# Optimization experiments

Hardware: AMD Instinct MI355X
Metric: run time of the kernel (lower is better)

## Reference

```python
import jax, jax.numpy as jnp
import numpy as np

B = 8192          # batch
D = 256           # feature_dim
H = 64            # num attention heads
HD = D // H       # head_dim = 4
NC, NB, NF, NT = 2048, 2048, 512, 768
NCLS = 26
EPS = 1e-5


def _linear_params(k, out_d, in_d):
    s = 1.0 / np.sqrt(in_d)
    kw, kb = jax.random.split(k)
    W = jax.random.uniform(kw, (out_d, in_d), minval=-s, maxval=s, dtype=jnp.float32)
    b = jax.random.uniform(kb, (out_d,), minval=-s, maxval=s, dtype=jnp.float32)
    return W, b


def setup_inputs() -> dict:
    key = jax.random.key(0)
    ks = jax.random.split(key, 16)
    inp = {
        'x_context': jax.random.normal(ks[0], (B, NC), dtype=jnp.float32),
        'x_body':    jax.random.normal(ks[1], (B, NB), dtype=jnp.float32),
        'x_face':    jax.random.normal(ks[2], (B, NF), dtype=jnp.float32),
        'x_text':    jax.random.normal(ks[3], (B, NT), dtype=jnp.float32),
    }
    inp['Wc'], inp['bc'] = _linear_params(ks[4], D, NC)
    inp['Wb'], inp['bb'] = _linear_params(ks[5], D, NB)
    inp['Wf'], inp['bf'] = _linear_params(ks[6], D, NF)
    inp['Wt'], inp['bt'] = _linear_params(ks[7], D, NT)
    # MultiheadAttention packed in-proj (3D x D) and out-proj
    inp['in_w'], inp['in_b'] = _linear_params(ks[8], 3 * D, D)
    inp['out_w'], inp['out_b'] = _linear_params(ks[9], D, D)
    # gate MLP
    inp['Wg1'], inp['bg1'] = _linear_params(ks[10], D, D)
    inp['Wg2'], inp['bg2'] = _linear_params(ks[11], 1, D)
    # fusion head
    inp['W1'], inp['b1'] = _linear_params(ks[12], D, 4 * D)
    inp['gamma'] = jnp.ones((D,), dtype=jnp.float32)
    inp['beta'] = jnp.zeros((D,), dtype=jnp.float32)
    inp['W2'], inp['b2'] = _linear_params(ks[13], NCLS, D)
    return inp


def reference(x_context, x_body, x_face, x_text,
              Wc, bc, Wb, bb, Wf, bf, Wt, bt,
              in_w, in_b, out_w, out_b,
              Wg1, bg1, Wg2, bg2,
              W1, b1, gamma, beta, W2, b2):
    # per-modality projections -> [B, 4, D]
    f = jnp.stack([
        x_context @ Wc.T + bc,
        x_body    @ Wb.T + bb,
        x_face    @ Wf.T + bf,
        x_text    @ Wt.T + bt,
    ], axis=1)
    bsz = f.shape[0]

    # MultiheadAttention with seq_len=1 per token: softmax over a single key
    Wq, Wk, Wv = jnp.split(in_w, 3, axis=0)
    bq, bk, bv = jnp.split(in_b, 3)
    q = (f @ Wq.T + bq).reshape(bsz, 4, H, HD)
    k = (f @ Wk.T + bk).reshape(bsz, 4, H, HD)
    v = (f @ Wv.T + bv).reshape(bsz, 4, H, HD)
    scores = jnp.sum(q * k, axis=-1, keepdims=True) / np.sqrt(HD)  # [B,4,H,1]
    w = jax.nn.softmax(scores, axis=-1)                            # == 1 (single key)
    attn = (w * v).reshape(bsz, 4, D)
    self_out = attn @ out_w.T + out_b                              # [B,4,D]

    # cross attention: with seq_len=1 the output depends only on key/value,
    # so each (query i, key 3-j) call equals the self-style output of modality 3-j;
    # combining over the 4 key variants reduces to the mean over modalities.
    cross = jnp.mean(self_out, axis=1, keepdims=True)              # [B,1,D]

    gate = jax.nn.sigmoid(jax.nn.relu(self_out @ Wg1.T + bg1) @ Wg2.T + bg2)  # [B,4,1]
    combined = gate * self_out + (1.0 - gate) * cross              # [B,4,D]

    h = combined.reshape(bsz, 4 * D) @ W1.T + b1                   # [B,D]
    # BatchNorm1d (training-mode batch statistics, biased variance)
    mu = jnp.mean(h, axis=0)
    var = jnp.var(h, axis=0)
    h = (h - mu) / jnp.sqrt(var + EPS) * gamma + beta
    h = jax.nn.relu(h)                                             # dropout = identity (eval)
    return h @ W2.T + b2                                           # [B,26]
```

## Files before the change

### kernel.cpp

```cpp
#include <hip/hip_runtime.h>
#include <math.h>

typedef __attribute__((ext_vector_type(8))) short bf16x8;
typedef __attribute__((ext_vector_type(4))) float f32x4;
typedef unsigned short u16;
typedef unsigned int u32;

#define BSZ   8192
#define BN_EPS 1e-5f

__device__ inline u16 f2bf(float x) {
    u32 u = __float_as_uint(x);
    u32 r = (u + 0x7FFFu + ((u >> 16) & 1u)) >> 16;
    return (u16)r;
}
__device__ inline float bf2f_lo(u32 p) { return __uint_as_float(p << 16); }
__device__ inline float bf2f_hi(u32 p) { return __uint_as_float(p & 0xFFFF0000u); }

__device__ inline void async_g2l(const void* g, void* l) {
    __builtin_amdgcn_global_load_lds(
        (const __attribute__((address_space(1))) void*)g,
        (__attribute__((address_space(3))) void*)l, 16, 0, 0);
}

__global__ __launch_bounds__(256)
void wvo_kernel(const float* __restrict__ in_w, const float* __restrict__ in_b,
                const float* __restrict__ out_w, const float* __restrict__ out_b,
                float* __restrict__ wvo, float* __restrict__ bvo)
{
    const int i = blockIdx.x;
    const int j = threadIdx.x;
    const float* Wv = in_w + 512 * 256;
    float s = 0.f;
#pragma unroll 8
    for (int k = 0; k < 256; ++k)
        s = fmaf(out_w[i * 256 + k], Wv[k * 256 + j], s);
    wvo[i * 256 + j] = s;
    if (i == 0) {
        const float* bv = in_b + 512;
        float t = 0.f;
        for (int k = 0; k < 256; ++k)
            t = fmaf(out_w[j * 256 + k], bv[k], t);
        bvo[j] = t + out_b[j];
    }
}

__global__ __launch_bounds__(256)
void cvt_weights(const float* __restrict__ wvo, const float* __restrict__ Wc,
                 const float* __restrict__ Wb,  const float* __restrict__ Wf,
                 const float* __restrict__ Wt,  const float* __restrict__ Wg1,
                 const float* __restrict__ W1f, u16* __restrict__ dst)
{
    int gid = blockIdx.x * 256 + threadIdx.x;
    const float* src; u16* d; int loc;
    if      (gid <   8192) { src = wvo; d = dst + 0;       loc = gid; }
    else if (gid <  73728) { src = Wc;  d = dst + 65536;   loc = gid - 8192; }
    else if (gid < 139264) { src = Wb;  d = dst + 589824;  loc = gid - 73728; }
    else if (gid < 155648) { src = Wf;  d = dst + 1114112; loc = gid - 139264; }
    else if (gid < 180224) { src = Wt;  d = dst + 1245184; loc = gid - 155648; }
    else if (gid < 188416) { src = Wg1; d = dst + 1441792; loc = gid - 180224; }
    else                   { src = W1f; d = dst + 1507328; loc = gid - 188416; }
    const float4 v0 = *(const float4*)(src + (size_t)loc * 8);
    const float4 v1 = *(const float4*)(src + (size_t)loc * 8 + 4);
    uint4 o;
    o.x = (u32)f2bf(v0.x) | ((u32)f2bf(v0.y) << 16);
    o.y = (u32)f2bf(v0.z) | ((u32)f2bf(v0.w) << 16);
    o.z = (u32)f2bf(v1.x) | ((u32)f2bf(v1.y) << 16);
    o.w = (u32)f2bf(v1.z) | ((u32)f2bf(v1.w) << 16);
    *(uint4*)(d + (size_t)loc * 8) = o;
}

__global__ __launch_bounds__(256)
void gemm_proj(const float* __restrict__ A0, const float* __restrict__ A1,
               const float* __restrict__ A2, const float* __restrict__ A3,
               const u16* __restrict__ Wp0, const u16* __restrict__ Wp1,
               const u16* __restrict__ Wp2, const u16* __restrict__ Wp3,
               const float* __restrict__ b0, const float* __restrict__ b1,
               const float* __restrict__ b2, const float* __restrict__ b3,
               u16* __restrict__ fb)
{
    __shared__ u16 As[2][4096];
    __shared__ u16 Bs[2][16384];
    const int m = blockIdx.y;
    const float* A  = (m == 0) ? A0 : (m == 1) ? A1 : (m == 2) ? A2 : A3;
    const u16* Wp   = (m == 0) ? Wp0 : (m == 1) ? Wp1 : (m == 2) ? Wp2 : Wp3;
    const float* bi = (m == 0) ? b0 : (m == 1) ? b1 : (m == 2) ? b2 : b3;
    const int K     = (m == 0) ? 2048 : (m == 1) ? 2048 : (m == 2) ? 512 : 768;
    const int nt = K >> 6;

    const int t = threadIdx.x;
    const int w = t >> 6, l = t & 63;
    const int bm = blockIdx.x * 64;
    const int arow = t >> 2, akq = t & 3;

    float4 rA[4], rB[4];
    auto loadA = [&](int k0, float4* r) {
        const float* g = A + (size_t)(bm + arow) * K + k0 + akq * 16;
#pragma unroll
        for (int q = 0; q < 4; ++q) r[q] = *(const float4*)(g + q * 4);
    };
    auto writeA = [&](int buf, const float4* r) {
        bf16x8 p0, p1;
        p0[0] = (short)f2bf(r[0].x); p0[1] = (short)f2bf(r[0].y);
        p0[2] = (short)f2bf(r[0].z); p0[3] = (short)f2bf(r[0].w);
        p0[4] = (short)f2bf(r[1].x); p0[5] = (short)f2bf(r[1].y);
        p0[6] = (short)f2bf(r[1].z); p0[7] = (short)f2bf(r[1].w);
        p1[0] = (short)f2bf(r[2].x); p1[1] = (short)f2bf(r[2].y);
        p1[2] = (short)f2bf(r[2].z); p1[3] = (short)f2bf(r[2].w);
        p1[4] = (short)f2bf(r[3].x); p1[5] = (short)f2bf(r[3].y);
        p1[6] = (short)f2bf(r[3].z); p1[7] = (short)f2bf(r[3].w);
        char* abw = (char*)As[buf];
        *(bf16x8*)(abw + arow * 128 + (((akq * 2 + 0) ^ (arow & 7)) << 4)) = p0;
        *(bf16x8*)(abw + arow * 128 + (((akq * 2 + 1) ^ (arow & 7)) << 4)) = p1;
    };
    auto issueB = [&](int k0, int buf) {
#pragma unroll
        for (int it = 0; it < 8; ++it) {
            const int n  = it * 32 + w * 8 + (l >> 3);
            const int ch = (l & 7) ^ (n & 7);
            async_g2l(Wp + (size_t)n * K + k0 + ch * 8, Bs[buf] + it * 2048 + w * 512);
        }
    };

    f32x4 acc[4][4];
    const f32x4 z = {0.f, 0.f, 0.f, 0.f};
#pragma unroll
    for (int i = 0; i < 4; ++i)
#pragma unroll
        for (int j = 0; j < 4; ++j) acc[i][j] = z;

    auto compute = [&](const char* abr, const char* bbr) {
#pragma unroll
        for (int kk = 0; kk < 2; ++kk) {
            bf16x8 af[4], bq[4];
            const int ch = kk * 4 + (l >> 4);
#pragma unroll
            for (int i = 0; i < 4; ++i) {
                const int fr = i * 16 + (l & 15);
                af[i] = *(const bf16x8*)(abr + fr * 128 + ((ch ^ (fr & 7)) << 4));
            }
#pragma unroll
            for (int j = 0; j < 4; ++j) {
                const int n = w * 64 + j * 16 + (l & 15);
                bq[j] = *(const bf16x8*)(bbr + n * 128 + ((ch ^ (n & 7)) << 4));
            }
#pragma unroll
            for (int i = 0; i < 4; ++i)
#pragma unroll
                for (int j = 0; j < 4; ++j)
                    acc[i][j] = __builtin_amdgcn_mfma_f32_16x16x32_bf16(
                        af[i], bq[j], acc[i][j], 0, 0, 0);
        }
    };

    loadA(0, rA);
    writeA(0, rA);
    issueB(0, 0);
    loadA(64, rB);
    issueB(64, 1);
    loadA(128, rA);
    asm volatile("s_waitcnt vmcnt(16) lgkmcnt(0)" ::: "memory");
    __builtin_amdgcn_sched_barrier(0);
    __builtin_amdgcn_s_barrier();

    for (int t0 = 0; t0 < nt; t0 += 2) {
        compute((const char*)As[0], (const char*)Bs[0]);
        writeA(1, rB);
        __builtin_amdgcn_s_barrier();
        if (t0 + 3 < nt) {
            loadA((t0 + 3) * 64, rB);
            issueB((t0 + 2) * 64, 0);
            asm volatile("s_waitcnt vmcnt(12) lgkmcnt(0)" ::: "memory");
        } else if (t0 + 2 < nt) {
            issueB((t0 + 2) * 64, 0);
            asm volatile("s_waitcnt vmcnt(8) lgkmcnt(0)" ::: "memory");
        } else {
            asm volatile("s_waitcnt vmcnt(0) lgkmcnt(0)" ::: "memory");
        }
        __builtin_amdgcn_sched_barrier(0);
        __builtin_amdgcn_s_barrier();

        compute((const char*)As[1], (const char*)Bs[1]);
        if (t0 + 2 < nt) writeA(0, rA);
        __builtin_amdgcn_s_barrier();
        if (t0 + 4 < nt) {
            loadA((t0 + 4) * 64, rA);
            issueB((t0 + 3) * 64, 1);
            asm volatile("s_waitcnt vmcnt(12) lgkmcnt(0)" ::: "memory");
        } else if (t0 + 3 < nt) {
            issueB((t0 + 3) * 64, 1);
            asm volatile("s_waitcnt vmcnt(8) lgkmcnt(0)" ::: "memory");
        } else {
            asm volatile("s_waitcnt vmcnt(0) lgkmcnt(0)" ::: "memory");
        }
        __builtin_amdgcn_sched_barrier(0);
        __builtin_amdgcn_s_barrier();
    }

#pragma unroll
    for (int j = 0; j < 4; ++j) {
        const int col = w * 64 + j * 16 + (l & 15);
        const float bv = bi[col];
#pragma unroll
        for (int i = 0; i < 4; ++i)
#pragma unroll
            for (int r = 0; r < 4; ++r) {
                const int rt = i * 16 + ((l >> 4) << 2) + r;
                fb[((size_t)(bm + rt) * 4 + m) * 256 + col] = f2bf(acc[i][j][r] + bv);
            }
    }
}

__global__ __launch_bounds__(256)
void fused_sgc(const u16* __restrict__ fb, const u16* __restrict__ wvo_bf,
               const float* __restrict__ bvo,
               const u16* __restrict__ wg1_bf, const float* __restrict__ bg1,
               const float* __restrict__ wg2, const float* __restrict__ bg2,
               u16* __restrict__ comb)
{
    __shared__ u16 FS[8192];
    __shared__ u16 Bs[2][8192];
    __shared__ float gp[4][32];
    __shared__ float gate_s[32];
    const int t = threadIdx.x, w = t >> 6, l = t & 63;
    const int bm = blockIdx.x * 32;
    char* const fs = (char*)FS;

#pragma unroll
    for (int it = 0; it < 4; ++it) {
        const int r0 = (w * 4 + it) * 2;
        const int row = r0 + (l >> 5);
        const int ch = (l & 31) ^ (row & 7);
        async_g2l(fb + (size_t)(bm + row) * 256 + ch * 8, FS + r0 * 256);
    }
    auto issueB = [&](const u16* Wp, int k0, int buf) {
#pragma unroll
        for (int it = 0; it < 4; ++it) {
            const int n0 = (w * 4 + it) * 16;
            async_g2l(Wp + (size_t)(n0 + (l >> 2)) * 256 + k0 + (l & 3) * 8,
                      Bs[buf] + n0 * 32);
        }
    };
    issueB(wvo_bf, 0, 0);
    __syncthreads();

    const f32x4 z = {0.f, 0.f, 0.f, 0.f};

    f32x4 acc[2][4];
#pragma unroll
    for (int i = 0; i < 2; ++i)
#pragma unroll
        for (int j = 0; j < 4; ++j) acc[i][j] = z;

    for (int ks = 0; ks < 8; ++ks) {
        const int cur = ks & 1;
        if (ks < 7) issueB(wvo_bf, (ks + 1) * 32, cur ^ 1);
        else        issueB(wg1_bf, 0, 0);
        bf16x8 af[2], bq[4];
#pragma unroll
        for (int i = 0; i < 2; ++i) {
            const int row = i * 16 + (l & 15);
            af[i] = *(const bf16x8*)(fs + row * 512 +
                      (((ks * 4 + (l >> 4)) ^ (row & 7)) << 4));
        }
#pragma unroll
        for (int j = 0; j < 4; ++j)
            bq[j] = *(const bf16x8*)((char*)Bs[cur] +
                      (w * 64 + j * 16 + (l & 15)) * 64 + (l >> 4) * 16);
#pragma unroll
        for (int i = 0; i < 2; ++i)
#pragma unroll
            for (int j = 0; j < 4; ++j)
                acc[i][j] = __builtin_amdgcn_mfma_f32_16x16x32_bf16(
                    af[i], bq[j], acc[i][j], 0, 0, 0);
        __syncthreads();
    }

#pragma unroll
    for (int j = 0; j < 4; ++j) {
        const int col = w * 64 + j * 16 + (l & 15);
        const float bv = bvo[col];
#pragma unroll
        for (int i = 0; i < 2; ++i)
#pragma unroll
            for (int r = 0; r < 4; ++r) {
                const int rt = i * 16 + ((l >> 4) << 2) + r;
                *(u16*)(fs + rt * 512 + (((col >> 3) ^ (rt & 7)) << 4) + (col & 7) * 2)
                    = f2bf(acc[i][j][r] + bv);
            }
    }
    __syncthreads();

    f32x4 g2[2][4];
#pragma unroll
    for (int i = 0; i < 2; ++i)
#pragma unroll
        for (int j = 0; j < 4; ++j) g2[i][j] = z;

    for (int ks = 0; ks < 8; ++ks) {
        const int cur = ks & 1;
        if (ks < 7) issueB(wg1_bf, (ks + 1) * 32, cur ^ 1);
        bf16x8 af[2], bq[4];
#pragma unroll
        for (int i = 0; i < 2; ++i) {
            const int row = i * 16 + (l & 15);
            af[i] = *(const bf16x8*)(fs + row * 512 +
                      (((ks * 4 + (l >> 4)) ^ (row & 7)) << 4));
        }
#pragma unroll
        for (int j = 0; j < 4; ++j)
            bq[j] = *(const bf16x8*)((char*)Bs[cur] +
                      (w * 64 + j * 16 + (l & 15)) * 64 + (l >> 4) * 16);
#pragma unroll
        for (int i = 0; i < 2; ++i)
#pragma unroll
            for (int j = 0; j < 4; ++j)
                g2[i][j] = __builtin_amdgcn_mfma_f32_16x16x32_bf16(
                    af[i], bq[j], g2[i][j], 0, 0, 0);
        __syncthreads();
    }

    {
        float s[2][4];
#pragma unroll
        for (int i = 0; i < 2; ++i)
#pragma unroll
            for (int r = 0; r < 4; ++r) s[i][r] = 0.f;
#pragma unroll
        for (int j = 0; j < 4; ++j) {
            const int col = w * 64 + j * 16 + (l & 15);
            const float bv = bg1[col], wv = wg2[col];
#pragma unroll
            for (int i = 0; i < 2; ++i)
#pragma unroll
                for (int r = 0; r < 4; ++r)
                    s[i][r] += fmaxf(g2[i][j][r] + bv, 0.f) * wv;
        }
#pragma unroll
        for (int off = 1; off < 16; off <<= 1)
#pragma unroll
            for (int i = 0; i < 2; ++i)
#pragma unroll
                for (int r = 0; r < 4; ++r)
                    s[i][r] += __shfl_xor(s[i][r], off);
        if ((l & 15) == 0) {
#pragma unroll
            for (int i = 0; i < 2; ++i)
#pragma unroll
                for (int r = 0; r < 4; ++r)
                    gp[w][i * 16 + ((l >> 4) << 2) + r] = s[i][r];
        }
    }
    __syncthreads();
    if (t < 32) {
        const float g = gp[0][t] + gp[1][t] + gp[2][t] + gp[3][t] + bg2[0];
        gate_s[t] = 1.f / (1.f + expf(-g));
    }
    __syncthreads();

    u32* const comb32 = (u32*)comb;
    const int p2 = t & 127;
    const int gh = t >> 7;
#pragma unroll
    for (int gg = 0; gg < 4; ++gg) {
        const int g = gh * 4 + gg;
        const int d0 = p2 * 2;
        float lo4[4], hi4[4], gv[4];
#pragma unroll
        for (int mm = 0; mm < 4; ++mm) {
            const int row = g * 4 + mm;
            const u32 v = *(const u32*)(fs + row * 512 +
                            (((d0 >> 3) ^ (row & 7)) << 4) + (d0 & 7) * 2);
            lo4[mm] = bf2f_lo(v); hi4[mm] = bf2f_hi(v);
            gv[mm] = gate_s[g * 4 + mm];
        }
        const float cl = 0.25f * (lo4[0] + lo4[1] + lo4[2] + lo4[3]);
        const float ch = 0.25f * (hi4[0] + hi4[1] + hi4[2] + hi4[3]);
#pragma unroll
        for (int mm = 0; mm < 4; ++mm) {
            const float ol = gv[mm] * lo4[mm] + (1.f - gv[mm]) * cl;
            const float oh = gv[mm] * hi4[mm] + (1.f - gv[mm]) * ch;
            comb32[(size_t)(bm + g * 4 + mm) * 128 + p2] =
                (u32)f2bf(ol) | ((u32)f2bf(oh) << 16);
        }
    }
}

__global__ __launch_bounds__(256)
void gemm_w1ps(const u16* __restrict__ combp, const u16* __restrict__ w1p,
               const float* __restrict__ b1p, float* __restrict__ h,
               float* __restrict__ psum, float* __restrict__ psq)
{
    __shared__ u16 As[2][1024];
    __shared__ u16 Bs[2][8192];
    const int t = threadIdx.x, w = t >> 6, l = t & 63;
    const int bm = blockIdx.x * 32;
    const int nt = 32;

    auto issueA = [&](int k0, int buf) {
        if (w < 2) {
            const int r0 = w * 16;
            async_g2l(combp + (size_t)(bm + r0 + (l >> 2)) * 1024 + k0 + (l & 3) * 8,
                      As[buf] + r0 * 32);
        }
    };
    auto issueB = [&](int k0, int buf) {
#pragma unroll
        for (int it = 0; it < 4; ++it) {
            const int n0 = (w * 4 + it) * 16;
            async_g2l(w1p + (size_t)(n0 + (l >> 2)) * 1024 + k0 + (l & 3) * 8,
                      Bs[buf] + n0 * 32);
        }
    };

    f32x4 acc[2][4];
    const f32x4 z = {0.f, 0.f, 0.f, 0.f};
#pragma unroll
    for (int i = 0; i < 2; ++i)
#pragma unroll
        for (int j = 0; j < 4; ++j) acc[i][j] = z;

    issueA(0, 0);
    issueB(0, 0);
    __syncthreads();

    for (int t0 = 0; t0 < nt; ++t0) {
        const int cur = t0 & 1;
        if (t0 + 1 < nt) { issueA((t0 + 1) * 32, cur ^ 1); issueB((t0 + 1) * 32, cur ^ 1); }
        const char* ab = (const char*)As[cur];
        const char* bb = (const char*)Bs[cur];
        bf16x8 af[2], bq[4];
#pragma unroll
        for (int i = 0; i < 2; ++i)
            af[i] = *(const bf16x8*)(ab + (i * 16 + (l & 15)) * 64 + (l >> 4) * 16);
#pragma unroll
        for (int j = 0; j < 4; ++j)
            bq[j] = *(const bf16x8*)(bb + (w * 64 + j * 16 + (l & 15)) * 64 + (l >> 4) * 16);
#pragma unroll
        for (int i = 0; i < 2; ++i)
#pragma unroll
            for (int j = 0; j < 4; ++j)
                acc[i][j] = __builtin_amdgcn_mfma_f32_16x16x32_bf16(
                    af[i], bq[j], acc[i][j], 0, 0, 0);
        __syncthreads();
    }

#pragma unroll
    for (int j = 0; j < 4; ++j) {
        const int col = w * 64 + j * 16 + (l & 15);
        const float bv = b1p[col];
        float cs = 0.f, cq = 0.f;
#pragma unroll
        for (int i = 0; i < 2; ++i)
#pragma unroll
            for (int r = 0; r < 4; ++r) {
                const int rt = i * 16 + ((l >> 4) << 2) + r;
                const float v = acc[i][j][r] + bv;
                h[(size_t)(bm + rt) * 256 + col] = v;
                cs += v;
                cq = fmaf(v, v, cq);
            }
        cs += __shfl_xor(cs, 16); cq += __shfl_xor(cq, 16);
        cs += __shfl_xor(cs, 32); cq += __shfl_xor(cq, 32);
        if ((l >> 4) == 0) {
            psum[blockIdx.x * 256 + col] = cs;
            psq[blockIdx.x * 256 + col]  = cq;
        }
    }
}

__global__ __launch_bounds__(256)
void bn_fin(const float* __restrict__ psum, const float* __restrict__ psq,
            const float* __restrict__ gamma, const float* __restrict__ beta,
            float* __restrict__ scale, float* __restrict__ shift)
{
    const int d = threadIdx.x;
    float s = 0.f, q = 0.f;
#pragma unroll 8
    for (int p = 0; p < 256; ++p) { s += psum[p * 256 + d]; q += psq[p * 256 + d]; }
    const float mu  = s * (1.f / BSZ);
    const float var = q * (1.f / BSZ) - mu * mu;
    const float inv = rsqrtf(var + BN_EPS);
    const float sc  = gamma[d] * inv;
    scale[d] = sc;
    shift[d] = beta[d] - mu * sc;
}

__global__ __launch_bounds__(256)
void final_kernel(const float* __restrict__ h, const float* __restrict__ scale,
                  const float* __restrict__ shift, const float* __restrict__ W2,
                  const float* __restrict__ b2, float* __restrict__ out)
{
    __shared__ float W2s[26][260];
    __shared__ float scs[256], shs[256];
    const int t = threadIdx.x;
    for (int u = t; u < 26 * 256; u += 256) {
        const int c = u >> 8, n = u & 255;
        W2s[c][(n >> 6) * 65 + (n & 63)] = W2[u];
    }
    scs[t] = scale[t];
    shs[t] = shift[t];
    __syncthreads();

    const int r = blockIdx.x * 64 + (t >> 2);
    const int p = t & 3;
    float acc[26];
#pragma unroll
    for (int c = 0; c < 26; ++c) acc[c] = 0.f;
    const float* hr = h + (size_t)r * 256 + p * 64;
#pragma unroll
    for (int i4 = 0; i4 < 16; ++i4) {
        const float4 v4 = *(const float4*)(hr + i4 * 4);
#pragma unroll
        for (int q = 0; q < 4; ++q) {
            const int i = i4 * 4 + q;
            const int n = p * 64 + i;
            const float vv = (q == 0) ? v4.x : (q == 1) ? v4.y : (q == 2) ? v4.z : v4.w;
            const float v = fmaxf(fmaf(vv, scs[n], shs[n]), 0.f);
            const int sw = p * 65 + i;
#pragma unroll
            for (int c = 0; c < 26; ++c)
                acc[c] = fmaf(v, W2s[c][sw], acc[c]);
        }
    }
#pragma unroll
    for (int off = 1; off < 4; off <<= 1)
#pragma unroll
        for (int c = 0; c < 26; ++c)
            acc[c] += __shfl_xor(acc[c], off);
    if (p == 0) {
#pragma unroll
        for (int c = 0; c < 26; ++c)
            out[(size_t)r * 26 + c] = acc[c] + b2[c];
    }
}

extern "C" void kernel_launch(void* const* d_in, const int* in_sizes, int n_in,
                              void* d_out, int out_size, void* d_ws, size_t ws_size,
                              hipStream_t stream)
{
    const float* x_ctx  = (const float*)d_in[0];
    const float* x_body = (const float*)d_in[1];
    const float* x_face = (const float*)d_in[2];
    const float* x_text = (const float*)d_in[3];
    const float* Wc = (const float*)d_in[4];  const float* bc = (const float*)d_in[5];
    const float* Wb = (const float*)d_in[6];  const float* bb = (const float*)d_in[7];
    const float* Wf = (const float*)d_in[8];  const float* bf = (const float*)d_in[9];
    const float* Wt = (const float*)d_in[10]; const float* bt = (const float*)d_in[11];
    const float* in_w  = (const float*)d_in[12]; const float* in_b  = (const float*)d_in[13];
    const float* out_w = (const float*)d_in[14]; const float* out_b = (const float*)d_in[15];
    const float* Wg1 = (const float*)d_in[16]; const float* bg1 = (const float*)d_in[17];
    const float* Wg2 = (const float*)d_in[18]; const float* bg2 = (const float*)d_in[19];
    const float* W1  = (const float*)d_in[20]; const float* b1  = (const float*)d_in[21];
    const float* gamma = (const float*)d_in[22]; const float* beta = (const float*)d_in[23];
    const float* W2  = (const float*)d_in[24]; const float* b2  = (const float*)d_in[25];

    char* wsb = (char*)d_ws;
    u16*   f_bf  = (u16*)(wsb + 0);
    u16*   comb  = f_bf;
    float* h     = (float*)(wsb + (16u << 20));
    u16*   wpb   = (u16*)(wsb + (32u << 20));
    float* wvo   = (float*)(wsb + (36u << 20));
    float* bvo   = (float*)(wsb + (36u << 20) + 262144);
    float* psum  = (float*)(wsb + (37u << 20));
    float* psq   = (float*)(wsb + (37u << 20) + 262144);
    float* scale = (float*)(wsb + (37u << 20) + 524288);
    float* shift = (float*)(wsb + (37u << 20) + 528384);

    u16* wvo_bf = wpb + 0;
    u16* wc_bf  = wpb + 65536;
    u16* wb_bf  = wpb + 589824;
    u16* wf_bf  = wpb + 1114112;
    u16* wt_bf  = wpb + 1245184;
    u16* wg1_bf = wpb + 1441792;
    u16* w1_bf  = wpb + 1507328;

    wvo_kernel<<<256, 256, 0, stream>>>(in_w, in_b, out_w, out_b, wvo, bvo);
    cvt_weights<<<864, 256, 0, stream>>>(wvo, Wc, Wb, Wf, Wt, Wg1, W1, wpb);

    gemm_proj<<<dim3(128, 4), 256, 0, stream>>>(x_ctx, x_body, x_face, x_text,
                                                wc_bf, wb_bf, wf_bf, wt_bf,
                                                bc, bb, bf, bt, f_bf);

    fused_sgc<<<1024, 256, 0, stream>>>(f_bf, wvo_bf, bvo, wg1_bf, bg1,
                                        Wg2, bg2, comb);

    gemm_w1ps<<<256, 256, 0, stream>>>(comb, w1_bf, b1, h, psum, psq);

    bn_fin<<<1, 256, 0, stream>>>(psum, psq, gamma, beta, scale, shift);
    final_kernel<<<128, 256, 0, stream>>>(h, scale, shift, W2, b2, (float*)d_out);
}
```

Baseline: 151.9 us.

## Fuse W1 GEMM and BN partial sums into the gate/combine kernel

The W1 projection and BatchNorm partial-sum computation now run inside the fused self-attention/gate kernel. The combined features stay in LDS instead of being written to global memory and reloaded by a separate GEMM kernel, and the partial-sum buffers grow to 1024 blocks. Each block now computes only 8 output rows with 16-row MFMAs, so half of every MFMA tile is wasted and each block streams the full W1 weight from global memory. bn_fin is parallelized across 256 blocks with a wave-shuffle reduction to handle the larger number of partial sums.

```diff
diff --git a/kernel.cpp b/kernel.cpp
--- a/kernel.cpp
+++ b/kernel.cpp
@@ -212,11 +212,13 @@
 }
 
 __global__ __launch_bounds__(256)
-void fused_sgc(const u16* __restrict__ fb, const u16* __restrict__ wvo_bf,
-               const float* __restrict__ bvo,
-               const u16* __restrict__ wg1_bf, const float* __restrict__ bg1,
-               const float* __restrict__ wg2, const float* __restrict__ bg2,
-               u16* __restrict__ comb)
+void fused_sgw1(const u16* __restrict__ fb, const u16* __restrict__ wvo_bf,
+                const float* __restrict__ bvo,
+                const u16* __restrict__ wg1_bf, const float* __restrict__ bg1,
+                const float* __restrict__ wg2, const float* __restrict__ bg2,
+                const u16* __restrict__ w1p, const float* __restrict__ b1p,
+                float* __restrict__ h, float* __restrict__ psum,
+                float* __restrict__ psq)
 {
     __shared__ u16 FS[8192];
     __shared__ u16 Bs[2][8192];
@@ -233,7 +235,7 @@
         const int ch = (l & 31) ^ (row & 7);
         async_g2l(fb + (size_t)(bm + row) * 256 + ch * 8, FS + r0 * 256);
     }
-    auto issueB = [&](const u16* Wp, int k0, int buf) {
+    auto issueB256 = [&](const u16* Wp, int k0, int buf) {
 #pragma unroll
         for (int it = 0; it < 4; ++it) {
             const int n0 = (w * 4 + it) * 16;
@@ -241,7 +243,15 @@
                       Bs[buf] + n0 * 32);
         }
     };
-    issueB(wvo_bf, 0, 0);
+    auto issueB1024 = [&](int k0, int buf) {
+#pragma unroll
+        for (int it = 0; it < 4; ++it) {
+            const int n0 = (w * 4 + it) * 16;
+            async_g2l(w1p + (size_t)(n0 + (l >> 2)) * 1024 + k0 + (l & 3) * 8,
+                      Bs[buf] + n0 * 32);
+        }
+    };
+    issueB256(wvo_bf, 0, 0);
     __syncthreads();
 
     const f32x4 z = {0.f, 0.f, 0.f, 0.f};
@@ -254,8 +264,8 @@
 
     for (int ks = 0; ks < 8; ++ks) {
         const int cur = ks & 1;
-        if (ks < 7) issueB(wvo_bf, (ks + 1) * 32, cur ^ 1);
-        else        issueB(wg1_bf, 0, 0);
+        if (ks < 7) issueB256(wvo_bf, (ks + 1) * 32, cur ^ 1);
+        else        issueB256(wg1_bf, 0, 0);
         bf16x8 af[2], bq[4];
 #pragma unroll
         for (int i = 0; i < 2; ++i) {
@@ -299,7 +309,8 @@
 
     for (int ks = 0; ks < 8; ++ks) {
         const int cur = ks & 1;
-        if (ks < 7) issueB(wg1_bf, (ks + 1) * 32, cur ^ 1);
+        if (ks < 7) issueB256(wg1_bf, (ks + 1) * 32, cur ^ 1);
+        else        issueB1024(0, 0);
         bf16x8 af[2], bq[4];
 #pragma unroll
         for (int i = 0; i < 2; ++i) {
@@ -358,113 +369,78 @@
     }
     __syncthreads();
 
-    u32* const comb32 = (u32*)comb;
-    const int p2 = t & 127;
-    const int gh = t >> 7;
-#pragma unroll
-    for (int gg = 0; gg < 4; ++gg) {
-        const int g = gh * 4 + gg;
-        const int d0 = p2 * 2;
-        float lo4[4], hi4[4], gv[4];
-#pragma unroll
-        for (int mm = 0; mm < 4; ++mm) {
-            const int row = g * 4 + mm;
-            const u32 v = *(const u32*)(fs + row * 512 +
-                            (((d0 >> 3) ^ (row & 7)) << 4) + (d0 & 7) * 2);
-            lo4[mm] = bf2f_lo(v); hi4[mm] = bf2f_hi(v);
-            gv[mm] = gate_s[g * 4 + mm];
-        }
-        const float cl = 0.25f * (lo4[0] + lo4[1] + lo4[2] + lo4[3]);
-        const float ch = 0.25f * (hi4[0] + hi4[1] + hi4[2] + hi4[3]);
-#pragma unroll
-        for (int mm = 0; mm < 4; ++mm) {
-            const float ol = gv[mm] * lo4[mm] + (1.f - gv[mm]) * cl;
-            const float oh = gv[mm] * hi4[mm] + (1.f - gv[mm]) * ch;
-            comb32[(size_t)(bm + g * 4 + mm) * 128 + p2] =
-                (u32)f2bf(ol) | ((u32)f2bf(oh) << 16);
-        }
-    }
-}
-
-__global__ __launch_bounds__(256)
-void gemm_w1ps(const u16* __restrict__ combp, const u16* __restrict__ w1p,
-               const float* __restrict__ b1p, float* __restrict__ h,
-               float* __restrict__ psum, float* __restrict__ psq)
-{
-    __shared__ u16 As[2][1024];
-    __shared__ u16 Bs[2][8192];
-    const int t = threadIdx.x, w = t >> 6, l = t & 63;
-    const int bm = blockIdx.x * 32;
-    const int nt = 32;
-
-    auto issueA = [&](int k0, int buf) {
-        if (w < 2) {
-            const int r0 = w * 16;
-            async_g2l(combp + (size_t)(bm + r0 + (l >> 2)) * 1024 + k0 + (l & 3) * 8,
-                      As[buf] + r0 * 32);
-        }
-    };
-    auto issueB = [&](int k0, int buf) {
-#pragma unroll
-        for (int it = 0; it < 4; ++it) {
-            const int n0 = (w * 4 + it) * 16;
-            async_g2l(w1p + (size_t)(n0 + (l >> 2)) * 1024 + k0 + (l & 3) * 8,
-                      Bs[buf] + n0 * 32);
-        }
-    };
-
-    f32x4 acc[2][4];
-    const f32x4 z = {0.f, 0.f, 0.f, 0.f};
-#pragma unroll
-    for (int i = 0; i < 2; ++i)
-#pragma unroll
-        for (int j = 0; j < 4; ++j) acc[i][j] = z;
-
-    issueA(0, 0);
-    issueB(0, 0);
-    __syncthreads();
-
-    for (int t0 = 0; t0 < nt; ++t0) {
+    {
+        const int p2 = t & 127;
+        const int gh = t >> 7;
+#pragma unroll
+        for (int gg = 0; gg < 4; ++gg) {
+            const int g = gh * 4 + gg;
+            const int d0 = p2 * 2;
+            float lo4[4], hi4[4], gv[4];
+#pragma unroll
+            for (int mm = 0; mm < 4; ++mm) {
+                const int row = g * 4 + mm;
+                const u32 v = *(const u32*)(fs + row * 512 +
+                                (((d0 >> 3) ^ (row & 7)) << 4) + (d0 & 7) * 2);
+                lo4[mm] = bf2f_lo(v); hi4[mm] = bf2f_hi(v);
+                gv[mm] = gate_s[g * 4 + mm];
+            }
+            const float cl = 0.25f * (lo4[0] + lo4[1] + lo4[2] + lo4[3]);
+            const float ch = 0.25f * (hi4[0] + hi4[1] + hi4[2] + hi4[3]);
+#pragma unroll
+            for (int mm = 0; mm < 4; ++mm) {
+                const int row = g * 4 + mm;
+                const float ol = gv[mm] * lo4[mm] + (1.f - gv[mm]) * cl;
+                const float oh = gv[mm] * hi4[mm] + (1.f - gv[mm]) * ch;
+                *(u32*)(fs + row * 512 + (((d0 >> 3) ^ (row & 7)) << 4) + (d0 & 7) * 2)
+                    = (u32)f2bf(ol) | ((u32)f2bf(oh) << 16);
+            }
+        }
+    }
+    __syncthreads();
+
+    f32x4 a4[4];
+#pragma unroll
+    for (int j = 0; j < 4; ++j) a4[j] = z;
+
+    for (int t0 = 0; t0 < 32; ++t0) {
         const int cur = t0 & 1;
-        if (t0 + 1 < nt) { issueA((t0 + 1) * 32, cur ^ 1); issueB((t0 + 1) * 32, cur ^ 1); }
-        const char* ab = (const char*)As[cur];
+        if (t0 + 1 < 32) issueB1024((t0 + 1) * 32, cur ^ 1);
+        const int frow = (l & 7) * 4 + (t0 >> 3);
+        const int chnk = (t0 & 7) * 4 + (l >> 4);
+        const bf16x8 af = *(const bf16x8*)(fs + frow * 512 +
+                            ((chnk ^ (frow & 7)) << 4));
         const char* bb = (const char*)Bs[cur];
-        bf16x8 af[2], bq[4];
-#pragma unroll
-        for (int i = 0; i < 2; ++i)
-            af[i] = *(const bf16x8*)(ab + (i * 16 + (l & 15)) * 64 + (l >> 4) * 16);
-#pragma unroll
-        for (int j = 0; j < 4; ++j)
-            bq[j] = *(const bf16x8*)(bb + (w * 64 + j * 16 + (l & 15)) * 64 + (l >> 4) * 16);
-#pragma unroll
-        for (int i = 0; i < 2; ++i)
-#pragma unroll
-            for (int j = 0; j < 4; ++j)
-                acc[i][j] = __builtin_amdgcn_mfma_f32_16x16x32_bf16(
-                    af[i], bq[j], acc[i][j], 0, 0, 0);
+#pragma unroll
+        for (int j = 0; j < 4; ++j) {
+            const bf16x8 bq = *(const bf16x8*)(bb +
+                                (w * 64 + j * 16 + (l & 15)) * 64 + (l >> 4) * 16);
+            a4[j] = __builtin_amdgcn_mfma_f32_16x16x32_bf16(af, bq, a4[j], 0, 0, 0);
+        }
         __syncthreads();
     }
 
+    const int hb = blockIdx.x * 8;
 #pragma unroll
     for (int j = 0; j < 4; ++j) {
         const int col = w * 64 + j * 16 + (l & 15);
         const float bv = b1p[col];
         float cs = 0.f, cq = 0.f;
-#pragma unroll
-        for (int i = 0; i < 2; ++i)
+        if (l < 32) {
 #pragma unroll
             for (int r = 0; r < 4; ++r) {
-                const int rt = i * 16 + ((l >> 4) << 2) + r;
-                const float v = acc[i][j][r] + bv;
-                h[(size_t)(bm + rt) * 256 + col] = v;
+                const int rt = ((l >> 4) << 2) + r;
+                const float v = a4[j][r] + bv;
+                h[(size_t)(hb + rt) * 256 + col] = v;
                 cs += v;
                 cq = fmaf(v, v, cq);
             }
+        }
         cs += __shfl_xor(cs, 16); cq += __shfl_xor(cq, 16);
         cs += __shfl_xor(cs, 32); cq += __shfl_xor(cq, 32);
         if ((l >> 4) == 0) {
-            psum[blockIdx.x * 256 + col] = cs;
-            psq[blockIdx.x * 256 + col]  = cq;
+            psum[(size_t)blockIdx.x * 256 + col] = cs;
+            psq[(size_t)blockIdx.x * 256 + col]  = cq;
         }
     }
 }
@@ -474,16 +450,33 @@
             const float* __restrict__ gamma, const float* __restrict__ beta,
             float* __restrict__ scale, float* __restrict__ shift)
 {
-    const int d = threadIdx.x;
+    __shared__ float ss[4], qq[4];
+    const int d = blockIdx.x;
+    const int t = threadIdx.x;
     float s = 0.f, q = 0.f;
-#pragma unroll 8
-    for (int p = 0; p < 256; ++p) { s += psum[p * 256 + d]; q += psq[p * 256 + d]; }
-    const float mu  = s * (1.f / BSZ);
-    const float var = q * (1.f / BSZ) - mu * mu;
-    const float inv = rsqrtf(var + BN_EPS);
-    const float sc  = gamma[d] * inv;
-    scale[d] = sc;
-    shift[d] = beta[d] - mu * sc;
+#pragma unroll
+    for (int u = 0; u < 4; ++u) {
+        const int p = u * 256 + t;
+        s += psum[(size_t)p * 256 + d];
+        q += psq[(size_t)p * 256 + d];
+    }
+#pragma unroll
+    for (int off = 1; off < 64; off <<= 1) {
+        s += __shfl_xor(s, off);
+        q += __shfl_xor(q, off);
+    }
+    if ((t & 63) == 0) { ss[t >> 6] = s; qq[t >> 6] = q; }
+    __syncthreads();
+    if (t == 0) {
+        s = ss[0] + ss[1] + ss[2] + ss[3];
+        q = qq[0] + qq[1] + qq[2] + qq[3];
+        const float mu  = s * (1.f / BSZ);
+        const float var = q * (1.f / BSZ) - mu * mu;
+        const float inv = rsqrtf(var + BN_EPS);
+        const float sc  = gamma[d] * inv;
+        scale[d] = sc;
+        shift[d] = beta[d] - mu * sc;
+    }
 }
 
 __global__ __launch_bounds__(256)
@@ -557,15 +550,14 @@
 
     char* wsb = (char*)d_ws;
     u16*   f_bf  = (u16*)(wsb + 0);
-    u16*   comb  = f_bf;
     float* h     = (float*)(wsb + (16u << 20));
     u16*   wpb   = (u16*)(wsb + (32u << 20));
     float* wvo   = (float*)(wsb + (36u << 20));
     float* bvo   = (float*)(wsb + (36u << 20) + 262144);
     float* psum  = (float*)(wsb + (37u << 20));
-    float* psq   = (float*)(wsb + (37u << 20) + 262144);
-    float* scale = (float*)(wsb + (37u << 20) + 524288);
-    float* shift = (float*)(wsb + (37u << 20) + 528384);
+    float* psq   = (float*)(wsb + (38u << 20));
+    float* scale = (float*)(wsb + (39u << 20));
+    float* shift = (float*)(wsb + (39u << 20) + 4096);
 
     u16* wvo_bf = wpb + 0;
     u16* wc_bf  = wpb + 65536;
@@ -582,11 +574,9 @@
                                                 wc_bf, wb_bf, wf_bf, wt_bf,
                                                 bc, bb, bf, bt, f_bf);
 
-    fused_sgc<<<1024, 256, 0, stream>>>(f_bf, wvo_bf, bvo, wg1_bf, bg1,
-                                        Wg2, bg2, comb);
-
-    gemm_w1ps<<<256, 256, 0, stream>>>(comb, w1_bf, b1, h, psum, psq);
-
-    bn_fin<<<1, 256, 0, stream>>>(psum, psq, gamma, beta, scale, shift);
+    fused_sgw1<<<1024, 256, 0, stream>>>(f_bf, wvo_bf, bvo, wg1_bf, bg1,
+                                         Wg2, bg2, w1_bf, b1, h, psum, psq);
+
+    bn_fin<<<256, 256, 0, stream>>>(psum, psq, gamma, beta, scale, shift);
     final_kernel<<<128, 256, 0, stream>>>(h, scale, shift, W2, b2, (float*)d_out);
 }
```

Measured after the change: 159.1 us. 4.8% more time.
